# Kernel tuning notes

Hardware: AMD Instinct MI355X
Metric: run time of the kernel (lower is better)

Reference implementation:

```python
import jax, jax.numpy as jnp
import numpy as np

N = 50000      # nodes
E = 800000     # edges (before self-loops)
IN = 256       # in_channels
H = 4          # heads (layer 1)
C = 64         # hidden per head
OUT = 40       # out_channels / classes


def setup_inputs() -> dict:
    key = jax.random.key(0)
    ks = jax.random.split(key, 10)
    s = 0.05  # weight init scale
    return {
        "x": jax.random.normal(ks[0], (N, IN), jnp.float32),
        "edge_index": jax.random.randint(ks[1], (2, E), 0, N),
        "W1": jax.random.normal(ks[2], (IN, H * C), jnp.float32) * s,
        "a_src1": jax.random.normal(ks[3], (H, C), jnp.float32) * s,
        "a_dst1": jax.random.normal(ks[4], (H, C), jnp.float32) * s,
        "b1": jnp.zeros((H * C,), jnp.float32),
        "W2": jax.random.normal(ks[5], (H * C, OUT), jnp.float32) * s,
        "a_src2": jax.random.normal(ks[6], (1, OUT), jnp.float32) * s,
        "a_dst2": jax.random.normal(ks[7], (1, OUT), jnp.float32) * s,
        "b2": jnp.zeros((OUT,), jnp.float32),
    }


def _gat_layer(x, src, dst, W, a_src, a_dst, bias, heads, out_c):
    """PyG GATConv (concat=True, negative_slope=0.2, self-loops already in src/dst)."""
    n = x.shape[0]
    h = (x @ W).reshape(n, heads, out_c)                    # [N,H,C]
    al_s = jnp.sum(h * a_src, axis=-1)                      # [N,H]
    al_d = jnp.sum(h * a_dst, axis=-1)                      # [N,H]
    e = jax.nn.leaky_relu(al_s[src] + al_d[dst], 0.2)       # [Etot,H]
    # edge softmax over incoming edges of each destination node
    m = jax.ops.segment_max(e, dst, num_segments=n)         # [N,H]
    ee = jnp.exp(e - m[dst])
    denom = jax.ops.segment_sum(ee, dst, num_segments=n)
    alpha = ee / (denom[dst] + 1e-16)                       # [Etot,H]
    msg = alpha[:, :, None] * h[src]                        # [Etot,H,C]
    out = jax.ops.segment_sum(msg, dst, num_segments=n)     # [N,H,C]
    return out.reshape(n, heads * out_c) + bias


def reference(x, edge_index, W1, a_src1, a_dst1, b1, W2, a_src2, a_dst2, b2):
    n = x.shape[0]
    loops = jnp.arange(n, dtype=edge_index.dtype)
    src = jnp.concatenate([edge_index[0], loops])
    dst = jnp.concatenate([edge_index[1], loops])
    h = _gat_layer(x, src, dst, W1, a_src1, a_dst1, b1, H, C)   # [N, H*C]
    h = jax.nn.relu(h)
    # F.dropout in eval mode is identity (reference run in eval mode)
    out = _gat_layer(h, src, dst, W2, a_src2, a_dst2, b2, 1, OUT)  # [N, OUT]
    return jax.nn.log_softmax(out, axis=1)
```

## Files before the change

### kernel.cpp

```cpp
#include <hip/hip_runtime.h>
#include <hip/hip_bf16.h>

typedef __hip_bfloat16 bf16;
typedef short v8s __attribute__((ext_vector_type(8)));
typedef float v4f __attribute__((ext_vector_type(4)));

constexpr int NN    = 50000;
constexpr int NE    = 800000;
constexpr int NETOT = 850000;
constexpr int CIN   = 256;
constexpr int HC    = 256;
constexpr int NH    = 4;
constexpr int NOUT  = 40;
constexpr int NPAD  = 48;
constexpr int SCB   = 196;

constexpr size_t al256(size_t x){ return (x + 255) & ~(size_t)255; }
constexpr size_t WS_FLAGS = 0;
constexpr size_t WS_EW1   = 256;
constexpr size_t WS_W1T   = al256(WS_EW1   + (size_t)NETOT*16);
constexpr size_t WS_AS1N  = al256(WS_W1T   + (size_t)CIN*HC*2);
constexpr size_t WS_AD1N  = al256(WS_AS1N  + HC*2);
constexpr size_t WS_B1N   = al256(WS_AD1N  + HC*2);
constexpr size_t WS_W2T   = al256(WS_B1N   + HC*2);
constexpr size_t WS_AS2N  = al256(WS_W2T   + (size_t)NPAD*HC*2);
constexpr size_t WS_AD2N  = al256(WS_AS2N  + NOUT*2);
constexpr size_t WS_B2N   = al256(WS_AD2N  + NOUT*2);
constexpr size_t WS_COUNTS= al256(WS_B2N   + NOUT*2);
constexpr size_t WS_CURSOR= al256(WS_COUNTS+ (size_t)NN*4);
constexpr size_t WS_ROWPTR= al256(WS_CURSOR+ (size_t)NN*4);
constexpr size_t WS_EPAIR = al256(WS_ROWPTR+ (size_t)(NN+1)*4);
constexpr size_t WS_H1    = al256(WS_EPAIR + (size_t)NETOT*8);
constexpr size_t WS_ALS1  = al256(WS_H1    + (size_t)NN*HC);
constexpr size_t WS_ALD1  = al256(WS_ALS1  + (size_t)NN*NH*4);
constexpr size_t WS_Y1    = al256(WS_ALD1  + (size_t)NN*NH*4);
constexpr size_t WS_H2    = al256(WS_Y1    + (size_t)NN*HC*2);
constexpr size_t WS_ALS2  = al256(WS_H2    + (size_t)NN*NOUT*2);
constexpr size_t WS_ALD2  = al256(WS_ALS2  + (size_t)NN*4);
constexpr size_t WS_EW2   = al256(WS_ALD2  + (size_t)NN*4);
constexpr size_t WS_BSUM  = al256(WS_EW2   + (size_t)NETOT*4);
constexpr size_t WS_BOFF  = al256(WS_BSUM  + 1024);

constexpr int CV_W1  = 0;
constexpr int CV_AS1 = CV_W1  + CIN*HC;
constexpr int CV_AD1 = CV_AS1 + HC;
constexpr int CV_B1  = CV_AD1 + HC;
constexpr int CV_W2  = CV_B1  + HC;
constexpr int CV_AS2 = CV_W2  + HC*NOUT;
constexpr int CV_AD2 = CV_AS2 + NOUT;
constexpr int CV_B2  = CV_AD2 + NOUT;
constexpr int CV_HIST= CV_B2  + NOUT;
constexpr int CV_END = CV_HIST + NE;

__device__ __forceinline__ float b2f(bf16 v) { return __bfloat162float(v); }
__device__ __forceinline__ bf16  f2b(float v){ return __float2bfloat16(v); }
__device__ __forceinline__ float bits2f(unsigned short u){ return __uint_as_float(((unsigned)u) << 16); }
__device__ __forceinline__ unsigned short f2bits(float v){
  bf16 t = __float2bfloat16(v);
  return *reinterpret_cast<unsigned short*>(&t);
}
__device__ __forceinline__ float lrelu(float x){ return x > 0.f ? x : 0.2f * x; }

__device__ __forceinline__ float wave_sum(float v){
  #pragma unroll
  for (int off = 32; off; off >>= 1) v += __shfl_xor(v, off, 64);
  return v;
}
__device__ __forceinline__ float wave_max(float v){
  #pragma unroll
  for (int off = 32; off; off >>= 1) v = fmaxf(v, __shfl_xor(v, off, 64));
  return v;
}

__global__ __launch_bounds__(64) void k_detect(const unsigned short* __restrict__ xu,
                                               const unsigned* __restrict__ eu,
                                               int* __restrict__ flags){
  int lane = threadIdx.x;
  int cnt = 0;
  for (int i = lane; i < 256; i += 64){
    int e = (xu[i] >> 7) & 0xFF;
    cnt += (e >= 0x60 && e <= 0x8F) ? 1 : 0;
  }
  #pragma unroll
  for (int off = 32; off; off >>= 1) cnt += __shfl_xor(cnt, off, 64);
  unsigned odd = eu[2 * lane + 1];
  #pragma unroll
  for (int off = 32; off; off >>= 1) odd |= __shfl_xor(odd, off, 64);
  if (lane == 0){
    flags[0] = (cnt < 218) ? 1 : 0;
    flags[1] = (odd == 0)  ? 1 : 0;
  }
}

__device__ __forceinline__ bf16 cvt_b(const void* src, int i, int f32m){
  if (f32m) return __float2bfloat16(((const float*)src)[i]);
  return ((const bf16*)src)[i];
}

__global__ __launch_bounds__(256) void k_convert(
    const void* __restrict__ W1,
    const void* __restrict__ as1,const void* __restrict__ ad1,
    const void* __restrict__ b1, const void* __restrict__ W2,
    const void* __restrict__ as2,const void* __restrict__ ad2,
    const void* __restrict__ b2, const void* __restrict__ ei,
    char* __restrict__ ws){
  const int* flags = (const int*)(ws + WS_FLAGS);
  int f32m = flags[0], i64m = flags[1];
  bf16* w1t  = (bf16*)(ws + WS_W1T);
  bf16* as1n = (bf16*)(ws + WS_AS1N);
  bf16* ad1n = (bf16*)(ws + WS_AD1N);
  bf16* b1n  = (bf16*)(ws + WS_B1N);
  bf16* w2t  = (bf16*)(ws + WS_W2T);
  bf16* as2n = (bf16*)(ws + WS_AS2N);
  bf16* ad2n = (bf16*)(ws + WS_AD2N);
  bf16* b2n  = (bf16*)(ws + WS_B2N);
  int*  counts=(int*) (ws + WS_COUNTS);
  for (int g = blockIdx.x * 256 + threadIdx.x; g < CV_END; g += gridDim.x * 256){
    if      (g < CV_AS1){ int i = g-CV_W1; int k = i >> 8, n = i & 255;
      w1t[n*CIN + k] = cvt_b(W1, i, f32m); }
    else if (g < CV_AD1) as1n[g-CV_AS1] = cvt_b(as1,g-CV_AS1, f32m);
    else if (g < CV_B1 ) ad1n[g-CV_AD1] = cvt_b(ad1,g-CV_AD1, f32m);
    else if (g < CV_W2 ) b1n [g-CV_B1 ] = cvt_b(b1, g-CV_B1,  f32m);
    else if (g < CV_AS2){ int i = g-CV_W2; int k = i / NOUT, n = i - k*NOUT;
      w2t[n*CIN + k] = cvt_b(W2, i, f32m); }
    else if (g < CV_AD2) as2n[g-CV_AS2] = cvt_b(as2,g-CV_AS2, f32m);
    else if (g < CV_B2 ) ad2n[g-CV_AD2] = cvt_b(ad2,g-CV_AD2, f32m);
    else if (g < CV_HIST) b2n[g-CV_B2 ] = cvt_b(b2, g-CV_B2,  f32m);
    else { int i = g-CV_HIST;
      int d = i64m ? (int)((const long long*)ei)[(size_t)NE+i] : ((const int*)ei)[NE+i];
      atomicAdd(&counts[d], 1); }
  }
}

__global__ __launch_bounds__(256) void k_scan_part(const int* __restrict__ counts, int* __restrict__ bsum){
  __shared__ int lds[256];
  int t = threadIdx.x;
  int idx = blockIdx.x * 256 + t;
  int v = (idx < NN) ? counts[idx] + 1 : 0;
  lds[t] = v;
  #pragma unroll
  for (int s = 128; s > 0; s >>= 1){
    __syncthreads();
    if (t < s) lds[t] += lds[t + s];
  }
  if (t == 0) bsum[blockIdx.x] = lds[0];
}

__global__ __launch_bounds__(256) void k_scan_mid(const int* __restrict__ bsum, int* __restrict__ boff,
                                                  int* __restrict__ row_ptr){
  __shared__ int lds[256];
  int t = threadIdx.x;
  int v = (t < SCB) ? bsum[t] : 0;
  lds[t] = v;
  for (int off = 1; off < 256; off <<= 1){
    __syncthreads();
    int u = (t >= off) ? lds[t - off] : 0;
    __syncthreads();
    lds[t] += u;
  }
  __syncthreads();
  if (t < SCB) boff[t] = lds[t] - v;
  if (t == 0) row_ptr[NN] = NETOT;
}

__global__ __launch_bounds__(256) void k_scan_apply(const int* __restrict__ counts, const int* __restrict__ boff,
                                                    int* __restrict__ row_ptr){
  __shared__ int lds[256];
  int t = threadIdx.x;
  int idx = blockIdx.x * 256 + t;
  int v = (idx < NN) ? counts[idx] + 1 : 0;
  lds[t] = v;
  for (int off = 1; off < 256; off <<= 1){
    __syncthreads();
    int u = (t >= off) ? lds[t - off] : 0;
    __syncthreads();
    lds[t] += u;
  }
  __syncthreads();
  if (idx < NN) row_ptr[idx] = boff[blockIdx.x] + lds[t] - v;
}

__global__ __launch_bounds__(256) void k_scatter(const void* __restrict__ ei, const int* __restrict__ flags,
                                                 const int* __restrict__ row_ptr,
                                                 int* __restrict__ cursor, int2* __restrict__ epair){
  int i = blockIdx.x * 256 + threadIdx.x;
  if (i >= NETOT) return;
  int s, d;
  if (i < NE){
    if (flags[1]){ s = (int)((const long long*)ei)[i]; d = (int)((const long long*)ei)[(size_t)NE + i]; }
    else         { s = ((const int*)ei)[i];            d = ((const int*)ei)[NE + i]; }
  } else { s = i - NE; d = i - NE; }
  int pos = row_ptr[d] + atomicAdd(&cursor[d], 1);
  epair[pos] = make_int2(s, d);
}

constexpr int G1R = 64;
constexpr int LP  = 72;
__global__ __launch_bounds__(256) void k_gemm1(const void* __restrict__ xin,
                                               const int* __restrict__ flags,
                                               const bf16* __restrict__ w1t,
                                               const bf16* __restrict__ as1, const bf16* __restrict__ ad1,
                                               unsigned char* __restrict__ h1q,
                                               float* __restrict__ al_s1, float* __restrict__ al_d1){
  __shared__ short Ab[G1R * LP];
  __shared__ short Bb[256 * LP];
  int tid  = threadIdx.x;
  int w    = tid >> 6, lane = tid & 63, quad = lane >> 4, c = lane & 15;
  int row0 = blockIdx.x * G1R;
  int f32m = flags[0];

  v4f acc[4][4];
  #pragma unroll
  for (int mt = 0; mt < 4; ++mt)
    #pragma unroll
    for (int nt = 0; nt < 4; ++nt) acc[mt][nt] = (v4f){0.f,0.f,0.f,0.f};

  int arow = tid >> 2;
  int aseg = tid & 3;
  int grow = row0 + arow; if (grow >= NN) grow = NN - 1;

  for (int ph = 0; ph < 4; ++ph){
    if (ph) __syncthreads();
    {
      short va[16];
      if (f32m){
        const float* src = (const float*)xin + (size_t)grow * CIN + ph*64 + aseg*16;
        #pragma unroll
        for (int i = 0; i < 4; ++i){
          float4 f = *reinterpret_cast<const float4*>(src + i*4);
          va[i*4+0] = (short)f2bits(f.x); va[i*4+1] = (short)f2bits(f.y);
          va[i*4+2] = (short)f2bits(f.z); va[i*4+3] = (short)f2bits(f.w);
        }
      } else {
        const short* src = (const short*)xin + (size_t)grow * CIN + ph*64 + aseg*16;
        v8s u0 = *reinterpret_cast<const v8s*>(src);
        v8s u1 = *reinterpret_cast<const v8s*>(src + 8);
        #pragma unroll
        for (int i = 0; i < 8; ++i){ va[i] = u0[i]; va[8+i] = u1[i]; }
      }
      short* dst = &Ab[arow * LP + aseg * 16];
      *reinterpret_cast<v8s*>(dst)     = *reinterpret_cast<v8s*>(&va[0]);
      *reinterpret_cast<v8s*>(dst + 8) = *reinterpret_cast<v8s*>(&va[8]);
    }
    {
      const short* src = (const short*)w1t + (size_t)tid * CIN + ph*64;
      short* dst = &Bb[tid * LP];
      #pragma unroll
      for (int j = 0; j < 8; ++j)
        *reinterpret_cast<v8s*>(dst + j*8) = *reinterpret_cast<const v8s*>(src + j*8);
    }
    __syncthreads();
    #pragma unroll
    for (int s = 0; s < 2; ++s){
      int ch = s*4 + quad;
      v8s af[4], bfb[4];
      #pragma unroll
      for (int mt = 0; mt < 4; ++mt)
        af[mt] = *reinterpret_cast<const v8s*>(&Ab[(mt*16 + c) * LP + ch*8]);
      #pragma unroll
      for (int nt = 0; nt < 4; ++nt)
        bfb[nt] = *reinterpret_cast<const v8s*>(&Bb[(w*64 + nt*16 + c) * LP + ch*8]);
      #pragma unroll
      for (int mt = 0; mt < 4; ++mt)
        #pragma unroll
        for (int nt = 0; nt < 4; ++nt)
          acc[mt][nt] = __builtin_amdgcn_mfma_f32_16x16x32_bf16(af[mt], bfb[nt], acc[mt][nt], 0, 0, 0);
    }
  }

  float as1v[4], ad1v[4];
  #pragma unroll
  for (int nt = 0; nt < 4; ++nt){
    as1v[nt] = b2f(as1[w*64 + nt*16 + c]);
    ad1v[nt] = b2f(ad1[w*64 + nt*16 + c]);
  }
  #pragma unroll
  for (int mt = 0; mt < 4; ++mt){
    #pragma unroll
    for (int r = 0; r < 4; ++r){
      float ps = 0.f, pd = 0.f;
      #pragma unroll
      for (int nt = 0; nt < 4; ++nt){ ps += acc[mt][nt][r] * as1v[nt]; pd += acc[mt][nt][r] * ad1v[nt]; }
      #pragma unroll
      for (int off = 1; off < 16; off <<= 1){ ps += __shfl_xor(ps, off, 64); pd += __shfl_xor(pd, off, 64); }
      int row = row0 + mt*16 + quad*4 + r;
      if (c == 0 && row < NN){
        al_s1[row * NH + w] = ps;
        al_d1[row * NH + w] = pd;
      }
    }
  }
  #pragma unroll
  for (int mt = 0; mt < 4; ++mt){
    #pragma unroll
    for (int nt = 0; nt < 4; ++nt){
      #pragma unroll
      for (int r = 0; r < 4; r += 2){
        int row = row0 + mt*16 + quad*4 + r;
        if (row + 1 < NN){
          int pk = __builtin_amdgcn_cvt_pk_fp8_f32(acc[mt][nt][r], acc[mt][nt][r+1], 0, false);
          size_t col = w*64 + nt*16 + c;
          h1q[(size_t)row       * HC + col] = (unsigned char)(pk & 0xFF);
          h1q[(size_t)(row + 1) * HC + col] = (unsigned char)((pk >> 8) & 0xFF);
        } else if (row < NN){
          int pk = __builtin_amdgcn_cvt_pk_fp8_f32(acc[mt][nt][r], acc[mt][nt][r], 0, false);
          h1q[(size_t)row * HC + w*64 + nt*16 + c] = (unsigned char)(pk & 0xFF);
        }
      }
    }
  }
}

__global__ __launch_bounds__(256) void k_ew1(const int2* __restrict__ epair,
                                             const float* __restrict__ al_s1, const float* __restrict__ al_d1,
                                             float4* __restrict__ ew1){
  int p = blockIdx.x * 256 + threadIdx.x;
  if (p >= NETOT) return;
  int2 pr = epair[p];
  float4 as = reinterpret_cast<const float4*>(al_s1)[pr.x];
  float4 ad = reinterpret_cast<const float4*>(al_d1)[pr.y];
  float4 w;
  w.x = __expf(lrelu(as.x + ad.x));
  w.y = __expf(lrelu(as.y + ad.y));
  w.z = __expf(lrelu(as.z + ad.z));
  w.w = __expf(lrelu(as.w + ad.w));
  ew1[p] = w;
}

__global__ __launch_bounds__(256) void k_gather1(const int* __restrict__ row_ptr, const int2* __restrict__ epair,
                                                 const float* __restrict__ ew1,
                                                 const unsigned* __restrict__ h1v, const bf16* __restrict__ b1,
                                                 bf16* __restrict__ y1){
  int lane = threadIdx.x & 63;
  int n = blockIdx.x * 4 + (threadIdx.x >> 6);
  int h = lane >> 4;
  int p0 = __builtin_amdgcn_readfirstlane(row_ptr[n]);
  int p1 = __builtin_amdgcn_readfirstlane(row_ptr[n + 1]);
  float den = 0.f, a0 = 0.f, a1 = 0.f, a2 = 0.f, a3 = 0.f;
  int p = p0;
  for (; p + 1 < p1; p += 2){
    int sA = __builtin_amdgcn_readfirstlane(epair[p].x);
    int sB = __builtin_amdgcn_readfirstlane(epair[p + 1].x);
    float wA = ew1[(size_t)p * 4 + h];
    float wB = ew1[(size_t)(p + 1) * 4 + h];
    unsigned uA = h1v[(size_t)sA * 64 + lane];
    unsigned uB = h1v[(size_t)sB * 64 + lane];
    den += wA + wB;
    a0 += wA * __builtin_amdgcn_cvt_f32_fp8(uA, 0) + wB * __builtin_amdgcn_cvt_f32_fp8(uB, 0);
    a1 += wA * __builtin_amdgcn_cvt_f32_fp8(uA, 1) + wB * __builtin_amdgcn_cvt_f32_fp8(uB, 1);
    a2 += wA * __builtin_amdgcn_cvt_f32_fp8(uA, 2) + wB * __builtin_amdgcn_cvt_f32_fp8(uB, 2);
    a3 += wA * __builtin_amdgcn_cvt_f32_fp8(uA, 3) + wB * __builtin_amdgcn_cvt_f32_fp8(uB, 3);
  }
  if (p < p1){
    int s = __builtin_amdgcn_readfirstlane(epair[p].x);
    float w = ew1[(size_t)p * 4 + h];
    unsigned u = h1v[(size_t)s * 64 + lane];
    den += w;
    a0 += w * __builtin_amdgcn_cvt_f32_fp8(u, 0);
    a1 += w * __builtin_amdgcn_cvt_f32_fp8(u, 1);
    a2 += w * __builtin_amdgcn_cvt_f32_fp8(u, 2);
    a3 += w * __builtin_amdgcn_cvt_f32_fp8(u, 3);
  }
  float inv = 1.f / (den + 1e-16f);
  ushort4 bb = reinterpret_cast<const ushort4*>(b1)[lane];
  ushort4 o;
  o.x = f2bits(fmaxf(a0 * inv + bits2f(bb.x), 0.f));
  o.y = f2bits(fmaxf(a1 * inv + bits2f(bb.y), 0.f));
  o.z = f2bits(fmaxf(a2 * inv + bits2f(bb.z), 0.f));
  o.w = f2bits(fmaxf(a3 * inv + bits2f(bb.w), 0.f));
  reinterpret_cast<ushort4*>(y1)[(size_t)n * 64 + lane] = o;
}

constexpr int W2LP = 260;
__global__ __launch_bounds__(256) void k_gemm2(const bf16* __restrict__ y1, const bf16* __restrict__ w2t,
                                               const bf16* __restrict__ as2, const bf16* __restrict__ ad2,
                                               bf16* __restrict__ h2, float* __restrict__ al_s2,
                                               float* __restrict__ al_d2){
  __shared__ short Wb[NPAD * W2LP];
  int tid = threadIdx.x;
  int w = tid >> 6, lane = tid & 63, quad = lane >> 4, c = lane & 15;
  int m0 = blockIdx.x * 64 + w * 16;
  for (int idx = tid; idx < NPAD * 32; idx += 256){
    int n = idx >> 5, sg = idx & 31;
    *reinterpret_cast<v8s*>(&Wb[n * W2LP + sg * 8]) =
      *reinterpret_cast<const v8s*>((const short*)w2t + (size_t)n * CIN + sg * 8);
  }
  int arow = m0 + c; if (arow >= NN) arow = NN - 1;
  const short* ar = (const short*)y1 + (size_t)arow * HC + quad * 8;
  v8s a[8];
  #pragma unroll
  for (int i = 0; i < 8; ++i) a[i] = *reinterpret_cast<const v8s*>(ar + i * 32);
  __syncthreads();

  v4f acc[3];
  #pragma unroll
  for (int t = 0; t < 3; ++t) acc[t] = (v4f){0.f, 0.f, 0.f, 0.f};
  #pragma unroll
  for (int k = 0; k < 8; ++k){
    int ch = k*4 + quad;
    #pragma unroll
    for (int t = 0; t < 3; ++t){
      v8s b = *reinterpret_cast<const v8s*>(&Wb[(t*16 + c) * W2LP + ch * 8]);
      acc[t] = __builtin_amdgcn_mfma_f32_16x16x32_bf16(a[k], b, acc[t], 0, 0, 0);
    }
  }
  float as2f[3], ad2f[3];
  #pragma unroll
  for (int t = 0; t < 3; ++t){
    int col = t*16 + c;
    as2f[t] = (col < NOUT) ? b2f(as2[col]) : 0.f;
    ad2f[t] = (col < NOUT) ? b2f(ad2[col]) : 0.f;
  }
  #pragma unroll
  for (int r = 0; r < 4; ++r){
    int row = m0 + quad*4 + r;
    float ps = 0.f, pd = 0.f;
    #pragma unroll
    for (int t = 0; t < 3; ++t){ ps += acc[t][r] * as2f[t]; pd += acc[t][r] * ad2f[t]; }
    #pragma unroll
    for (int off = 1; off < 16; off <<= 1){ ps += __shfl_xor(ps, off, 64); pd += __shfl_xor(pd, off, 64); }
    if (row < NN){
      if (c == 0){ al_s2[row] = ps; al_d2[row] = pd; }
      #pragma unroll
      for (int t = 0; t < 3; ++t){
        int col = t*16 + c;
        if (col < NOUT) h2[(size_t)row * NOUT + col] = f2b(acc[t][r]);
      }
    }
  }
}

__global__ __launch_bounds__(256) void k_ew2(const int2* __restrict__ epair,
                                             const float* __restrict__ al_s2, const float* __restrict__ al_d2,
                                             float* __restrict__ ew2){
  int p = blockIdx.x * 256 + threadIdx.x;
  if (p >= NETOT) return;
  int2 pr = epair[p];
  ew2[p] = __expf(lrelu(al_s2[pr.x] + al_d2[pr.y]));
}

__global__ __launch_bounds__(256) void k_gather2(const int* __restrict__ row_ptr, const int2* __restrict__ epair,
                                                 const float* __restrict__ ew2,
                                                 const bf16* __restrict__ h2, const bf16* __restrict__ b2v,
                                                 const int* __restrict__ flags, void* __restrict__ out){
  int lane = threadIdx.x & 63;
  int n = blockIdx.x * 4 + (threadIdx.x >> 6);
  int p0 = __builtin_amdgcn_readfirstlane(row_ptr[n]);
  int p1 = __builtin_amdgcn_readfirstlane(row_ptr[n + 1]);
  float den = 0.f, acc = 0.f;
  int p = p0;
  for (; p + 1 < p1; p += 2){
    int sA = __builtin_amdgcn_readfirstlane(epair[p].x);
    int sB = __builtin_amdgcn_readfirstlane(epair[p + 1].x);
    float wA = ew2[p], wB = ew2[p + 1];
    float hA = 0.f, hB = 0.f;
    if (lane < NOUT){
      hA = b2f(h2[(size_t)sA * NOUT + lane]);
      hB = b2f(h2[(size_t)sB * NOUT + lane]);
    }
    den += wA + wB;
    acc += wA * hA + wB * hB;
  }
  if (p < p1){
    int s = __builtin_amdgcn_readfirstlane(epair[p].x);
    float w = ew2[p];
    den += w;
    if (lane < NOUT) acc += w * b2f(h2[(size_t)s * NOUT + lane]);
  }
  float v = (lane < NOUT) ? (acc / (den + 1e-16f) + b2f(b2v[lane])) : -INFINITY;
  float M = wave_max(v);
  float ex = (lane < NOUT) ? __expf(v - M) : 0.f;
  float S = wave_sum(ex);
  if (lane < NOUT){
    float r = v - M - __logf(S);
    size_t idx = (size_t)n * NOUT + lane;
    if (flags[0]) ((float*)out)[idx] = r;
    else          ((bf16*)out)[idx]  = f2b(r);
  }
}

extern "C" void kernel_launch(void* const* d_in, const int* in_sizes, int n_in,
                              void* d_out, int out_size, void* d_ws, size_t ws_size,
                              hipStream_t stream) {
  const void* x   = d_in[0];
  const void* ei  = d_in[1];
  const void* W1  = d_in[2];
  const void* as1 = d_in[3];
  const void* ad1 = d_in[4];
  const void* b1  = d_in[5];
  const void* W2  = d_in[6];
  const void* as2 = d_in[7];
  const void* ad2 = d_in[8];
  const void* b2  = d_in[9];

  char* ws = (char*)d_ws;
  int*   flags   = (int*)  (ws + WS_FLAGS);
  float* ew1     = (float*)(ws + WS_EW1);
  bf16*  w1t     = (bf16*) (ws + WS_W1T);
  bf16*  as1n    = (bf16*) (ws + WS_AS1N);
  bf16*  ad1n    = (bf16*) (ws + WS_AD1N);
  bf16*  b1n     = (bf16*) (ws + WS_B1N);
  bf16*  w2t     = (bf16*) (ws + WS_W2T);
  bf16*  as2n    = (bf16*) (ws + WS_AS2N);
  bf16*  ad2n    = (bf16*) (ws + WS_AD2N);
  bf16*  b2n     = (bf16*) (ws + WS_B2N);
  int*   counts  = (int*)  (ws + WS_COUNTS);
  int*   cursor  = (int*)  (ws + WS_CURSOR);
  int*   row_ptr = (int*)  (ws + WS_ROWPTR);
  int2*  epair   = (int2*) (ws + WS_EPAIR);
  unsigned char* h1q = (unsigned char*)(ws + WS_H1);
  float* al_s1   = (float*)(ws + WS_ALS1);
  float* al_d1   = (float*)(ws + WS_ALD1);
  bf16*  y1      = (bf16*) (ws + WS_Y1);
  bf16*  h2      = (bf16*) (ws + WS_H2);
  float* al_s2   = (float*)(ws + WS_ALS2);
  float* al_d2   = (float*)(ws + WS_ALD2);
  float* ew2     = (float*)(ws + WS_EW2);
  int*   bsum    = (int*)  (ws + WS_BSUM);
  int*   boff    = (int*)  (ws + WS_BOFF);

  hipMemsetAsync(counts, 0, (size_t)NN * 4, stream);
  hipMemsetAsync(cursor, 0, (size_t)NN * 4, stream);
  hipMemsetAsync(w2t,    0, (size_t)NPAD * CIN * 2, stream);

  k_detect <<<1, 64, 0, stream>>>((const unsigned short*)x, (const unsigned*)ei, flags);
  k_convert<<<1024, 256, 0, stream>>>(W1, as1, ad1, b1, W2, as2, ad2, b2, ei, ws);

  int eb = (NETOT + 255) / 256;
  k_scan_part <<<SCB, 256, 0, stream>>>(counts, bsum);
  k_scan_mid  <<<1, 256, 0, stream>>>(bsum, boff, row_ptr);
  k_scan_apply<<<SCB, 256, 0, stream>>>(counts, boff, row_ptr);
  k_scatter<<<eb, 256, 0, stream>>>(ei, flags, row_ptr, cursor, epair);

  k_gemm1  <<<(NN + G1R - 1) / G1R, 256, 0, stream>>>(x, flags, w1t, as1n, ad1n, h1q, al_s1, al_d1);
  k_ew1    <<<eb, 256, 0, stream>>>(epair, al_s1, al_d1, (float4*)ew1);
  k_gather1<<<NN / 4, 256, 0, stream>>>(row_ptr, epair, ew1, (const unsigned*)h1q, b1n, y1);
  k_gemm2  <<<(NN + 63) / 64, 256, 0, stream>>>(y1, w2t, as2n, ad2n, h2, al_s2, al_d2);
  k_ew2    <<<eb, 256, 0, stream>>>(epair, al_s2, al_d2, ew2);
  k_gather2<<<NN / 4, 256, 0, stream>>>(row_ptr, epair, ew2, h2, b2n, flags, d_out);
}
```

Before: 341.5 us.

## Drop explicit self-loop edges from CSR and store source index only

Self-loops are no longer materialized in the CSR. Each gather kernel now seeds its accumulator with the node's own self-loop term. The per-edge pair array is shrunk to a source-only index array, and the edge-weight kernels are restructured as per-node wave loops that read al_d once per destination. This cuts scatter traffic, index bytes and the edge count, at the cost of less uniform per-wave work in the ew kernels.

```diff
diff --git a/kernel.cpp b/kernel.cpp
--- a/kernel.cpp
+++ b/kernel.cpp
@@ -7,7 +7,6 @@
 
 constexpr int NN    = 50000;
 constexpr int NE    = 800000;
-constexpr int NETOT = 850000;
 constexpr int CIN   = 256;
 constexpr int HC    = 256;
 constexpr int NH    = 4;
@@ -18,7 +17,7 @@
 constexpr size_t al256(size_t x){ return (x + 255) & ~(size_t)255; }
 constexpr size_t WS_FLAGS = 0;
 constexpr size_t WS_EW1   = 256;
-constexpr size_t WS_W1T   = al256(WS_EW1   + (size_t)NETOT*16);
+constexpr size_t WS_W1T   = al256(WS_EW1   + (size_t)NE*16);
 constexpr size_t WS_AS1N  = al256(WS_W1T   + (size_t)CIN*HC*2);
 constexpr size_t WS_AD1N  = al256(WS_AS1N  + HC*2);
 constexpr size_t WS_B1N   = al256(WS_AD1N  + HC*2);
@@ -29,8 +28,8 @@
 constexpr size_t WS_COUNTS= al256(WS_B2N   + NOUT*2);
 constexpr size_t WS_CURSOR= al256(WS_COUNTS+ (size_t)NN*4);
 constexpr size_t WS_ROWPTR= al256(WS_CURSOR+ (size_t)NN*4);
-constexpr size_t WS_EPAIR = al256(WS_ROWPTR+ (size_t)(NN+1)*4);
-constexpr size_t WS_H1    = al256(WS_EPAIR + (size_t)NETOT*8);
+constexpr size_t WS_EIDX  = al256(WS_ROWPTR+ (size_t)(NN+1)*4);
+constexpr size_t WS_H1    = al256(WS_EIDX  + (size_t)NE*4);
 constexpr size_t WS_ALS1  = al256(WS_H1    + (size_t)NN*HC);
 constexpr size_t WS_ALD1  = al256(WS_ALS1  + (size_t)NN*NH*4);
 constexpr size_t WS_Y1    = al256(WS_ALD1  + (size_t)NN*NH*4);
@@ -38,7 +37,7 @@
 constexpr size_t WS_ALS2  = al256(WS_H2    + (size_t)NN*NOUT*2);
 constexpr size_t WS_ALD2  = al256(WS_ALS2  + (size_t)NN*4);
 constexpr size_t WS_EW2   = al256(WS_ALD2  + (size_t)NN*4);
-constexpr size_t WS_BSUM  = al256(WS_EW2   + (size_t)NETOT*4);
+constexpr size_t WS_BSUM  = al256(WS_EW2   + (size_t)NE*4);
 constexpr size_t WS_BOFF  = al256(WS_BSUM  + 1024);
 
 constexpr int CV_W1  = 0;
@@ -136,7 +135,7 @@
   __shared__ int lds[256];
   int t = threadIdx.x;
   int idx = blockIdx.x * 256 + t;
-  int v = (idx < NN) ? counts[idx] + 1 : 0;
+  int v = (idx < NN) ? counts[idx] : 0;
   lds[t] = v;
   #pragma unroll
   for (int s = 128; s > 0; s >>= 1){
@@ -160,7 +159,7 @@
   }
   __syncthreads();
   if (t < SCB) boff[t] = lds[t] - v;
-  if (t == 0) row_ptr[NN] = NETOT;
+  if (t == 0) row_ptr[NN] = NE;
 }
 
 __global__ __launch_bounds__(256) void k_scan_apply(const int* __restrict__ counts, const int* __restrict__ boff,
@@ -168,7 +167,7 @@
   __shared__ int lds[256];
   int t = threadIdx.x;
   int idx = blockIdx.x * 256 + t;
-  int v = (idx < NN) ? counts[idx] + 1 : 0;
+  int v = (idx < NN) ? counts[idx] : 0;
   lds[t] = v;
   for (int off = 1; off < 256; off <<= 1){
     __syncthreads();
@@ -182,16 +181,14 @@
 
 __global__ __launch_bounds__(256) void k_scatter(const void* __restrict__ ei, const int* __restrict__ flags,
                                                  const int* __restrict__ row_ptr,
-                                                 int* __restrict__ cursor, int2* __restrict__ epair){
+                                                 int* __restrict__ cursor, int* __restrict__ eidx){
   int i = blockIdx.x * 256 + threadIdx.x;
-  if (i >= NETOT) return;
+  if (i >= NE) return;
   int s, d;
-  if (i < NE){
-    if (flags[1]){ s = (int)((const long long*)ei)[i]; d = (int)((const long long*)ei)[(size_t)NE + i]; }
-    else         { s = ((const int*)ei)[i];            d = ((const int*)ei)[NE + i]; }
-  } else { s = i - NE; d = i - NE; }
+  if (flags[1]){ s = (int)((const long long*)ei)[i]; d = (int)((const long long*)ei)[(size_t)NE + i]; }
+  else         { s = ((const int*)ei)[i];            d = ((const int*)ei)[NE + i]; }
   int pos = row_ptr[d] + atomicAdd(&cursor[d], 1);
-  epair[pos] = make_int2(s, d);
+  eidx[pos] = s;
 }
 
 constexpr int G1R = 64;
@@ -311,24 +308,29 @@
   }
 }
 
-__global__ __launch_bounds__(256) void k_ew1(const int2* __restrict__ epair,
+__global__ __launch_bounds__(256) void k_ew1(const int* __restrict__ row_ptr, const int* __restrict__ eidx,
                                              const float* __restrict__ al_s1, const float* __restrict__ al_d1,
                                              float4* __restrict__ ew1){
-  int p = blockIdx.x * 256 + threadIdx.x;
-  if (p >= NETOT) return;
-  int2 pr = epair[p];
-  float4 as = reinterpret_cast<const float4*>(al_s1)[pr.x];
-  float4 ad = reinterpret_cast<const float4*>(al_d1)[pr.y];
-  float4 w;
-  w.x = __expf(lrelu(as.x + ad.x));
-  w.y = __expf(lrelu(as.y + ad.y));
-  w.z = __expf(lrelu(as.z + ad.z));
-  w.w = __expf(lrelu(as.w + ad.w));
-  ew1[p] = w;
-}
-
-__global__ __launch_bounds__(256) void k_gather1(const int* __restrict__ row_ptr, const int2* __restrict__ epair,
+  int lane = threadIdx.x & 63;
+  int n = blockIdx.x * 4 + (threadIdx.x >> 6);
+  int p0 = __builtin_amdgcn_readfirstlane(row_ptr[n]);
+  int p1 = __builtin_amdgcn_readfirstlane(row_ptr[n + 1]);
+  float4 ad = reinterpret_cast<const float4*>(al_d1)[n];
+  for (int p = p0 + lane; p < p1; p += 64){
+    int s = eidx[p];
+    float4 as = reinterpret_cast<const float4*>(al_s1)[s];
+    float4 w;
+    w.x = __expf(lrelu(as.x + ad.x));
+    w.y = __expf(lrelu(as.y + ad.y));
+    w.z = __expf(lrelu(as.z + ad.z));
+    w.w = __expf(lrelu(as.w + ad.w));
+    ew1[p] = w;
+  }
+}
+
+__global__ __launch_bounds__(256) void k_gather1(const int* __restrict__ row_ptr, const int* __restrict__ eidx,
                                                  const float* __restrict__ ew1,
+                                                 const float* __restrict__ al_s1, const float* __restrict__ al_d1,
                                                  const unsigned* __restrict__ h1v, const bf16* __restrict__ b1,
                                                  bf16* __restrict__ y1){
   int lane = threadIdx.x & 63;
@@ -336,11 +338,17 @@
   int h = lane >> 4;
   int p0 = __builtin_amdgcn_readfirstlane(row_ptr[n]);
   int p1 = __builtin_amdgcn_readfirstlane(row_ptr[n + 1]);
-  float den = 0.f, a0 = 0.f, a1 = 0.f, a2 = 0.f, a3 = 0.f;
+  float wss = __expf(lrelu(al_s1[n * NH + h] + al_d1[n * NH + h]));
+  unsigned us = h1v[(size_t)n * 64 + lane];
+  float den = wss;
+  float a0 = wss * __builtin_amdgcn_cvt_f32_fp8(us, 0);
+  float a1 = wss * __builtin_amdgcn_cvt_f32_fp8(us, 1);
+  float a2 = wss * __builtin_amdgcn_cvt_f32_fp8(us, 2);
+  float a3 = wss * __builtin_amdgcn_cvt_f32_fp8(us, 3);
   int p = p0;
   for (; p + 1 < p1; p += 2){
-    int sA = __builtin_amdgcn_readfirstlane(epair[p].x);
-    int sB = __builtin_amdgcn_readfirstlane(epair[p + 1].x);
+    int sA = __builtin_amdgcn_readfirstlane(eidx[p]);
+    int sB = __builtin_amdgcn_readfirstlane(eidx[p + 1]);
     float wA = ew1[(size_t)p * 4 + h];
     float wB = ew1[(size_t)(p + 1) * 4 + h];
     unsigned uA = h1v[(size_t)sA * 64 + lane];
@@ -352,7 +360,7 @@
     a3 += wA * __builtin_amdgcn_cvt_f32_fp8(uA, 3) + wB * __builtin_amdgcn_cvt_f32_fp8(uB, 3);
   }
   if (p < p1){
-    int s = __builtin_amdgcn_readfirstlane(epair[p].x);
+    int s = __builtin_amdgcn_readfirstlane(eidx[p]);
     float w = ew1[(size_t)p * 4 + h];
     unsigned u = h1v[(size_t)s * 64 + lane];
     den += w;
@@ -430,28 +438,34 @@
   }
 }
 
-__global__ __launch_bounds__(256) void k_ew2(const int2* __restrict__ epair,
+__global__ __launch_bounds__(256) void k_ew2(const int* __restrict__ row_ptr, const int* __restrict__ eidx,
                                              const float* __restrict__ al_s2, const float* __restrict__ al_d2,
                                              float* __restrict__ ew2){
-  int p = blockIdx.x * 256 + threadIdx.x;
-  if (p >= NETOT) return;
-  int2 pr = epair[p];
-  ew2[p] = __expf(lrelu(al_s2[pr.x] + al_d2[pr.y]));
-}
-
-__global__ __launch_bounds__(256) void k_gather2(const int* __restrict__ row_ptr, const int2* __restrict__ epair,
+  int lane = threadIdx.x & 63;
+  int n = blockIdx.x * 4 + (threadIdx.x >> 6);
+  int p0 = __builtin_amdgcn_readfirstlane(row_ptr[n]);
+  int p1 = __builtin_amdgcn_readfirstlane(row_ptr[n + 1]);
+  float ad = al_d2[n];
+  for (int p = p0 + lane; p < p1; p += 64)
+    ew2[p] = __expf(lrelu(al_s2[eidx[p]] + ad));
+}
+
+__global__ __launch_bounds__(256) void k_gather2(const int* __restrict__ row_ptr, const int* __restrict__ eidx,
                                                  const float* __restrict__ ew2,
+                                                 const float* __restrict__ al_s2, const float* __restrict__ al_d2,
                                                  const bf16* __restrict__ h2, const bf16* __restrict__ b2v,
                                                  const int* __restrict__ flags, void* __restrict__ out){
   int lane = threadIdx.x & 63;
   int n = blockIdx.x * 4 + (threadIdx.x >> 6);
   int p0 = __builtin_amdgcn_readfirstlane(row_ptr[n]);
   int p1 = __builtin_amdgcn_readfirstlane(row_ptr[n + 1]);
-  float den = 0.f, acc = 0.f;
+  float wss = __expf(lrelu(al_s2[n] + al_d2[n]));
+  float den = wss;
+  float acc = (lane < NOUT) ? wss * b2f(h2[(size_t)n * NOUT + lane]) : 0.f;
   int p = p0;
   for (; p + 1 < p1; p += 2){
-    int sA = __builtin_amdgcn_readfirstlane(epair[p].x);
-    int sB = __builtin_amdgcn_readfirstlane(epair[p + 1].x);
+    int sA = __builtin_amdgcn_readfirstlane(eidx[p]);
+    int sB = __builtin_amdgcn_readfirstlane(eidx[p + 1]);
     float wA = ew2[p], wB = ew2[p + 1];
     float hA = 0.f, hB = 0.f;
     if (lane < NOUT){
@@ -462,7 +476,7 @@
     acc += wA * hA + wB * hB;
   }
   if (p < p1){
-    int s = __builtin_amdgcn_readfirstlane(epair[p].x);
+    int s = __builtin_amdgcn_readfirstlane(eidx[p]);
     float w = ew2[p];
     den += w;
     if (lane < NOUT) acc += w * b2f(h2[(size_t)s * NOUT + lane]);
@@ -507,7 +521,7 @@
   int*   counts  = (int*)  (ws + WS_COUNTS);
   int*   cursor  = (int*)  (ws + WS_CURSOR);
   int*   row_ptr = (int*)  (ws + WS_ROWPTR);
-  int2*  epair   = (int2*) (ws + WS_EPAIR);
+  int*   eidx    = (int*)  (ws + WS_EIDX);
   unsigned char* h1q = (unsigned char*)(ws + WS_H1);
   float* al_s1   = (float*)(ws + WS_ALS1);
   float* al_d1   = (float*)(ws + WS_ALD1);
@@ -526,16 +540,16 @@
   k_detect <<<1, 64, 0, stream>>>((const unsigned short*)x, (const unsigned*)ei, flags);
   k_convert<<<1024, 256, 0, stream>>>(W1, as1, ad1, b1, W2, as2, ad2, b2, ei, ws);
 
-  int eb = (NETOT + 255) / 256;
+  int eb = (NE + 255) / 256;
   k_scan_part <<<SCB, 256, 0, stream>>>(counts, bsum);
   k_scan_mid  <<<1, 256, 0, stream>>>(bsum, boff, row_ptr);
   k_scan_apply<<<SCB, 256, 0, stream>>>(counts, boff, row_ptr);
-  k_scatter<<<eb, 256, 0, stream>>>(ei, flags, row_ptr, cursor, epair);
+  k_scatter<<<eb, 256, 0, stream>>>(ei, flags, row_ptr, cursor, eidx);
 
   k_gemm1  <<<(NN + G1R - 1) / G1R, 256, 0, stream>>>(x, flags, w1t, as1n, ad1n, h1q, al_s1, al_d1);
-  k_ew1    <<<eb, 256, 0, stream>>>(epair, al_s1, al_d1, (float4*)ew1);
-  k_gather1<<<NN / 4, 256, 0, stream>>>(row_ptr, epair, ew1, (const unsigned*)h1q, b1n, y1);
+  k_ew1    <<<NN / 4, 256, 0, stream>>>(row_ptr, eidx, al_s1, al_d1, (float4*)ew1);
+  k_gather1<<<NN / 4, 256, 0, stream>>>(row_ptr, eidx, ew1, al_s1, al_d1, (const unsigned*)h1q, b1n, y1);
   k_gemm2  <<<(NN + 63) / 64, 256, 0, stream>>>(y1, w2t, as2n, ad2n, h2, al_s2, al_d2);
-  k_ew2    <<<eb, 256, 0, stream>>>(epair, al_s2, al_d2, ew2);
-  k_gather2<<<NN / 4, 256, 0, stream>>>(row_ptr, epair, ew2, h2, b2n, flags, d_out);
-}
+  k_ew2    <<<NN / 4, 256, 0, stream>>>(row_ptr, eidx, al_s2, al_d2, ew2);
+  k_gather2<<<NN / 4, 256, 0, stream>>>(row_ptr, eidx, ew2, al_s2, al_d2, h2, b2n, flags, d_out);
+}
```

New measurement: 342.5 us. About the same (+0.3%).
